# Optimization experiments

Hardware: AMD Instinct MI355X
Metric: run time of the kernel (lower is better)

## Reference

```python
import jax, jax.numpy as jnp
import numpy as np

N_HEADS = 8
D_HEAD = 64
INNER = N_HEADS * D_HEAD  # 512
D_X = 512
D_CTX = 768

def setup_inputs() -> dict:
    key = jax.random.key(0)
    ks = jax.random.split(key, 7)
    x = jax.random.normal(ks[0], (4, 4096, D_X), dtype=jnp.float32)
    context = jax.random.normal(ks[1], (4, 1024, D_CTX), dtype=jnp.float32)
    # Glorot-ish scaled params
    Wq = jax.random.normal(ks[2], (D_X, INNER), dtype=jnp.float32) / np.sqrt(D_X)
    Wk = jax.random.normal(ks[3], (D_CTX, INNER), dtype=jnp.float32) / np.sqrt(D_CTX)
    Wv = jax.random.normal(ks[4], (D_CTX, INNER), dtype=jnp.float32) / np.sqrt(D_CTX)
    Wo = jax.random.normal(ks[5], (INNER, INNER), dtype=jnp.float32) / np.sqrt(INNER)
    bo = jnp.zeros((INNER,), dtype=jnp.float32)
    return {"x": x, "context": context, "Wq": Wq, "Wk": Wk, "Wv": Wv, "Wo": Wo, "bo": bo}

def reference(x, context, Wq, Wk, Wv, Wo, bo):
    B, Nq, _ = x.shape
    Nc = context.shape[1]
    scale = D_HEAD ** -0.5
    # QKV projections (no bias), reshape to heads: b s (h d) -> b h s d
    q = (x @ Wq).reshape(B, Nq, N_HEADS, D_HEAD).transpose(0, 2, 1, 3)
    k = (context @ Wk).reshape(B, Nc, N_HEADS, D_HEAD).transpose(0, 2, 1, 3)
    v = (context @ Wv).reshape(B, Nc, N_HEADS, D_HEAD).transpose(0, 2, 1, 3)
    # scores: [B, H, Nq, Nc]
    score = jnp.einsum('bhqd,bhkd->bhqk', q, k) * scale
    weights = jax.nn.softmax(score, axis=-1)
    attn = jnp.einsum('bhqk,bhkd->bhqd', weights, v)
    out = attn.transpose(0, 2, 1, 3).reshape(B, Nq, INNER)
    return out @ Wo + bo
```

## Files before the change

### kernel.cpp

```cpp
#include <hip/hip_runtime.h>
#include <math.h>

typedef __attribute__((ext_vector_type(8))) short s8v;
typedef __attribute__((ext_vector_type(4))) float f4v;
typedef unsigned short u16;
typedef unsigned int u32;

constexpr int Bsz = 4, NQ = 4096, NC = 1024, NH = 8, DH = 64, DI = 512, DC = 768;

__device__ __forceinline__ u16 f2bf(float f) {
  union { float f; u32 u; } v; v.f = f;
  u32 r = v.u + 0x7fff + ((v.u >> 16) & 1);
  return (u16)(r >> 16);
}

__device__ __forceinline__ u32 pack2(float a, float b) {
  union { float f; u32 u; } ua, ub; ua.f = a; ub.f = b;
#if __has_builtin(__builtin_amdgcn_perm)
  return __builtin_amdgcn_perm(ub.u + 0x8000u, ua.u + 0x8000u, 0x07060302u);
#else
  return ((ub.u + 0x8000u) & 0xffff0000u) | ((ua.u + 0x8000u) >> 16);
#endif
}

__device__ __forceinline__ u32 cvtpk(float a, float b) {
  u32 r;
  asm("v_cvt_pk_bf16_f32 %0, %1, %2" : "=v"(r) : "v"(a), "v"(b));
  return r;
}

#if __has_builtin(__builtin_amdgcn_exp2f)
#define EXP2(x) __builtin_amdgcn_exp2f(x)
#else
#define EXP2(x) exp2f(x)
#endif

__device__ __forceinline__ void g2l16(const void* g, void* l) {
  __builtin_amdgcn_global_load_lds((const __attribute__((address_space(1))) u32*)g,
                                   (__attribute__((address_space(3))) u32*)l, 16, 0, 0);
}

__global__ __launch_bounds__(256) void prep(const float* __restrict__ Wq, const float* __restrict__ Wk,
                                            const float* __restrict__ Wv, const float* __restrict__ Wo,
                                            u16* __restrict__ wqT, u16* __restrict__ wkvT,
                                            u16* __restrict__ woT) {
  int idx = blockIdx.x;
  int z = idx / 96, rem = idx % 96, kx = rem % 12, ny = rem / 12;
  const float* src; u16* dst; int K; const int N = 512;
  if (z == 0)      { src = Wq; dst = wqT;              K = 512; }
  else if (z == 1) { src = Wk; dst = wkvT;             K = 768; }
  else if (z == 2) { src = Wv; dst = wkvT + 512 * 768; K = 768; }
  else             { src = Wo; dst = woT;              K = 512; }
  int k0 = kx * 64, n0 = ny * 64;
  if (k0 >= K) return;
  __shared__ u16 t[64][65];
  int tid = threadIdx.x, jr = tid & 63, ir = tid >> 6;
  for (int it = 0; it < 16; ++it) { int i = it * 4 + ir; t[i][jr] = f2bf(src[(size_t)(k0 + i) * N + n0 + jr]); }
  __syncthreads();
  for (int it = 0; it < 16; ++it) { int i = it * 4 + ir; dst[(size_t)(n0 + i) * K + k0 + jr] = t[jr][i]; }
}

template <int MODE, bool F32A>
__device__ __forceinline__ void gemm_body(const void* __restrict__ Av, const u16* __restrict__ Bt,
                                          void* __restrict__ C0, void* __restrict__ C1,
                                          const float* __restrict__ bias, int N, int K,
                                          float oscale, int nbx, int mby,
                                          u16* Al, u16* Bl) {
  int mb = mby * 128, nb = nbx * 128;
  int tid = threadIdx.x, lane = tid & 63, quad = lane >> 4, l16 = lane & 15, wave = tid >> 6;
  int wm = (wave >> 1) * 64, wn = (wave & 1) * 64;
  f4v acc[4][4];
  #pragma unroll
  for (int i = 0; i < 4; i++)
    #pragma unroll
    for (int j = 0; j < 4; j++) acc[i][j] = (f4v){0.f, 0.f, 0.f, 0.f};

  int r0 = tid >> 2;
  int cs = ((tid & 3) ^ ((r0 >> 1) & 3)) * 8;
  int lin = tid * 8;
  const u16* Bp0 = Bt + (size_t)(nb + r0) * K + cs;
  const u16* Bp1 = Bp0 + (size_t)64 * K;
  const float* Af0 = nullptr; const float* Af1 = nullptr;
  const u16* Ap0 = nullptr; const u16* Ap1 = nullptr;
  if constexpr (F32A) {
    Af0 = (const float*)Av + (size_t)(mb + r0) * K + cs;
    Af1 = Af0 + (size_t)64 * K;
  } else {
    Ap0 = (const u16*)Av + (size_t)(mb + r0) * K + cs;
    Ap1 = Ap0 + (size_t)64 * K;
  }
  float4 ra[4], rb[4];

#define BSTG(k0, bl_) do { g2l16(Bp0 + (k0), (bl_) + lin); g2l16(Bp1 + (k0), (bl_) + lin + 2048); } while (0)
#define ASTG(k0, al_) do { g2l16(Ap0 + (k0), (al_) + lin); g2l16(Ap1 + (k0), (al_) + lin + 2048); } while (0)
#define ALD(k0, s) do { \
    s[0] = *(const float4*)(Af0 + (k0)); s[1] = *(const float4*)(Af0 + (k0) + 4); \
    s[2] = *(const float4*)(Af1 + (k0)); s[3] = *(const float4*)(Af1 + (k0) + 4); } while (0)
#define AWR(s, al_) do { union { u32 d[4]; s8v v; } ua, ub; \
    ua.d[0] = cvtpk(s[0].x, s[0].y); ua.d[1] = cvtpk(s[0].z, s[0].w); \
    ua.d[2] = cvtpk(s[1].x, s[1].y); ua.d[3] = cvtpk(s[1].z, s[1].w); \
    ub.d[0] = cvtpk(s[2].x, s[2].y); ub.d[1] = cvtpk(s[2].z, s[2].w); \
    ub.d[2] = cvtpk(s[3].x, s[3].y); ub.d[3] = cvtpk(s[3].z, s[3].w); \
    *(s8v*)((al_) + lin) = ua.v; *(s8v*)((al_) + lin + 2048) = ub.v; } while (0)

  u16 *Ar = Al, *Aw = Al + 4096, *As = Al + 8192;
  u16 *Br = Bl, *Bw = Bl + 4096, *Bs = Bl + 8192;
  if constexpr (F32A) {
    ALD(0, ra); BSTG(0, Br); AWR(ra, Ar);
    ALD(32, rb); BSTG(32, Bw);
  } else {
    ASTG(0, Ar); BSTG(0, Br);
    ASTG(32, Aw); BSTG(32, Bw);
  }

  int nk = K >> 5;
  int swq8 = (quad ^ ((l16 >> 1) & 3)) * 8;
  for (int t = 0; t < nk; ++t) {
    if (t + 1 < nk) {
      if constexpr (F32A) asm volatile("s_waitcnt vmcnt(6) lgkmcnt(0)" ::: "memory");
      else                asm volatile("s_waitcnt vmcnt(4) lgkmcnt(0)" ::: "memory");
    } else {
      asm volatile("s_waitcnt vmcnt(0) lgkmcnt(0)" ::: "memory");
    }
    __builtin_amdgcn_s_barrier();
    asm volatile("" ::: "memory");
    __builtin_amdgcn_sched_barrier(0);

    if (t + 2 < nk) {
      int nxt = (t + 2) * 32;
      if constexpr (F32A) {
        if (t & 1) { ALD(nxt, rb); } else { ALD(nxt, ra); }
        BSTG(nxt, Bs);
      } else {
        ASTG(nxt, As); BSTG(nxt, Bs);
      }
    }

    s8v af[4], bfr[4];
    #pragma unroll
    for (int i = 0; i < 4; i++) af[i] = *(const s8v*)(Ar + (wm + i * 16 + l16) * 32 + swq8);
    #pragma unroll
    for (int j = 0; j < 4; j++) bfr[j] = *(const s8v*)(Br + (wn + j * 16 + l16) * 32 + swq8);
    #pragma unroll
    for (int i = 0; i < 4; i++)
      #pragma unroll
      for (int j = 0; j < 4; j++)
        acc[i][j] = __builtin_amdgcn_mfma_f32_16x16x32_bf16(af[i], bfr[j], acc[i][j], 0, 0, 0);

    if constexpr (F32A) {
      if (t + 1 < nk) {
        if (t & 1) { AWR(ra, Aw); } else { AWR(rb, Aw); }
      }
    }
    u16* tA = Ar; Ar = Aw; Aw = As; As = tA;
    u16* tB = Br; Br = Bw; Bw = Bs; Bs = tB;
  }
#undef BSTG
#undef ASTG
#undef ALD
#undef AWR
  #pragma unroll
  for (int i = 0; i < 4; i++) {
    int rbase = mb + wm + i * 16 + quad * 4;
    #pragma unroll
    for (int j = 0; j < 4; j++) {
      int col = nb + wn + j * 16 + l16;
      if (MODE == 0) {
        u16* Cb = (u16*)C0;
        #pragma unroll
        for (int r = 0; r < 4; r++) Cb[(size_t)(rbase + r) * N + col] = f2bf(acc[i][j][r] * oscale);
      } else if (MODE == 1) {
        float* Cf = (float*)C0;
        #pragma unroll
        for (int r = 0; r < 4; r++) Cf[(size_t)(rbase + r) * N + col] = acc[i][j][r] + bias[col];
      } else {
        if (col < 512) {
          u16* Kb = (u16*)C0;
          #pragma unroll
          for (int r = 0; r < 4; r++) Kb[(size_t)(rbase + r) * 512 + col] = f2bf(acc[i][j][r]);
        } else {
          u16* Vt = (u16*)C1;
          int hd = col - 512, h = hd >> 6, d = hd & 63;
          int bb = rbase >> 10, tl = rbase & 1023;
          int tbase = tl & ~63, a0 = tl & 63;
          int pb = (a0 & 32) + ((a0 & 15) >> 2) * 8 + (((a0 >> 4) & 1) << 2);
          uint2 ov;
          ov.x = pack2(acc[i][j][0], acc[i][j][1]);
          ov.y = pack2(acc[i][j][2], acc[i][j][3]);
          *(uint2*)(Vt + ((size_t)(bb * NH + h) * DH + d) * NC + tbase + pb) = ov;
        }
      }
    }
  }
}

__global__ __launch_bounds__(256, 3) void proj_all(const float* __restrict__ x, const float* __restrict__ ctx,
                                                   const u16* __restrict__ wqT, const u16* __restrict__ wkvT,
                                                   u16* __restrict__ Qb, u16* __restrict__ Kb,
                                                   u16* __restrict__ Vtb, float qscale) {
  __shared__ alignas(16) u16 Al[3][128][32];
  __shared__ alignas(16) u16 Bl[3][128][32];
  int bx = blockIdx.x;
  int xcd = bx & 7, off = bx >> 3;
  if (off < 32) {
    int bi = xcd * 32 + off;
    gemm_body<2, true>(ctx, wkvT, Kb, Vtb, nullptr, 1024, 768, 1.0f, bi & 7, bi >> 3,
                       (u16*)Al, (u16*)Bl);
  } else {
    int bi = xcd * 64 + (off - 32);
    gemm_body<0, true>(x, wqT, Qb, nullptr, nullptr, 512, 512, qscale, bi & 3, bi >> 2,
                       (u16*)Al, (u16*)Bl);
  }
}

__global__ __launch_bounds__(256, 3) void outproj(const u16* __restrict__ Ob, const u16* __restrict__ woT,
                                                  float* __restrict__ out, const float* __restrict__ bo) {
  __shared__ alignas(16) u16 Al[3][128][32];
  __shared__ alignas(16) u16 Bl[3][128][32];
  int bx = blockIdx.x;
  int idx = (bx & 7) * 64 + (bx >> 3);
  gemm_body<1, false>(Ob, woT, out, nullptr, bo, 512, 512, 1.0f, idx & 3, idx >> 2,
                      (u16*)Al, (u16*)Bl);
}

__global__ __launch_bounds__(256, 4) void attn(const u16* __restrict__ Q, const u16* __restrict__ Kb,
                                               const u16* __restrict__ Vt, u16* __restrict__ O) {
  __shared__ alignas(16) u16 Kl[2][64][64];
  __shared__ alignas(16) u16 Vl[2][64][64];
  int qt = blockIdx.x, h = blockIdx.y, b = blockIdx.z;
  int tid = threadIdx.x, wave = tid >> 6, lane = tid & 63, quad = lane >> 4, l16 = lane & 15;
  int q0 = qt * 128 + wave * 32;
  int x7 = l16 & 7;

  int kr = tid >> 3, kc = (tid & 7) ^ (kr & 7);
  const u16* kg = Kb + ((size_t)b * NC + kr) * 512 + h * DH + kc * 8;
  const u16* vg = Vt + ((size_t)(b * NH + h) * DH + kr) * NC + kc * 8;

#define ASTAGE(kt, buf) do { \
    const u16* kg_ = kg + (size_t)(kt) * 64 * 512; \
    const u16* vg_ = vg + (kt) * 64; \
    u16* kl_ = (u16*)Kl + (buf) * 4096; u16* vl_ = (u16*)Vl + (buf) * 4096; \
    g2l16(kg_,            kl_ + tid * 8); \
    g2l16(kg_ + 32 * 512, kl_ + (tid + 256) * 8); \
    g2l16(vg_,            vl_ + tid * 8); \
    g2l16(vg_ + 32 * NC,  vl_ + (tid + 256) * 8); } while (0)

  s8v aq[2][2];
  {
    const u16* Qp = Q + ((size_t)b * NQ + q0 + l16) * DI + h * DH + quad * 8;
    #pragma unroll
    for (int n = 0; n < 2; n++) {
      aq[n][0] = *(const s8v*)(Qp + (size_t)n * 16 * DI);
      aq[n][1] = *(const s8v*)(Qp + (size_t)n * 16 * DI + 32);
    }
  }
  s8v vones;
  #pragma unroll
  for (int i = 0; i < 8; i++) vones[i] = (short)0x3F80;

  f4v oacc[4][2];
  f4v lacc[2];
  #pragma unroll
  for (int d = 0; d < 4; d++)
    #pragma unroll
    for (int n = 0; n < 2; n++) oacc[d][n] = (f4v){0.f, 0.f, 0.f, 0.f};
  #pragma unroll
  for (int n = 0; n < 2; n++) lacc[n] = (f4v){0.f, 0.f, 0.f, 0.f};

  ASTAGE(0, 0);
  for (int kt = 0; kt < NC / 64; ++kt) {
    int buf = kt & 1;
    __syncthreads();
    if (kt + 1 < NC / 64) ASTAGE(kt + 1, buf ^ 1);
    const u16* kb = (const u16*)Kl + buf * 4096;
    const u16* vb = (const u16*)Vl + buf * 4096;

    f4v S0[2][2], S1[2][2];
    #pragma unroll
    for (int mi = 0; mi < 2; mi++)
      #pragma unroll
      for (int n = 0; n < 2; n++) { S0[mi][n] = (f4v){0.f,0.f,0.f,0.f}; S1[mi][n] = (f4v){0.f,0.f,0.f,0.f}; }
    __builtin_amdgcn_s_setprio(1);
    #pragma unroll
    for (int cd = 0; cd < 2; cd++) {
      int ch = ((4 * cd + quad) ^ x7) * 8;
      s8v k00 = *(const s8v*)(kb + (l16     ) * 64 + ch);
      s8v k01 = *(const s8v*)(kb + (l16 + 16) * 64 + ch);
      #pragma unroll
      for (int n = 0; n < 2; n++) {
        S0[0][n] = __builtin_amdgcn_mfma_f32_16x16x32_bf16(k00, aq[n][cd], S0[0][n], 0, 0, 0);
        S0[1][n] = __builtin_amdgcn_mfma_f32_16x16x32_bf16(k01, aq[n][cd], S0[1][n], 0, 0, 0);
      }
      s8v k10 = *(const s8v*)(kb + (l16 + 32) * 64 + ch);
      s8v k11 = *(const s8v*)(kb + (l16 + 48) * 64 + ch);
      #pragma unroll
      for (int n = 0; n < 2; n++) {
        S1[0][n] = __builtin_amdgcn_mfma_f32_16x16x32_bf16(k10, aq[n][cd], S1[0][n], 0, 0, 0);
        S1[1][n] = __builtin_amdgcn_mfma_f32_16x16x32_bf16(k11, aq[n][cd], S1[1][n], 0, 0, 0);
      }
    }
    __builtin_amdgcn_s_setprio(0);

    s8v pf0[2];
    #pragma unroll
    for (int n = 0; n < 2; n++) {
      float p00 = EXP2(S0[0][n][0]), p01 = EXP2(S0[0][n][1]), p02 = EXP2(S0[0][n][2]), p03 = EXP2(S0[0][n][3]);
      float p10 = EXP2(S0[1][n][0]), p11 = EXP2(S0[1][n][1]), p12 = EXP2(S0[1][n][2]), p13 = EXP2(S0[1][n][3]);
      union { u32 d[4]; s8v v; } u;
      u.d[0] = cvtpk(p00, p01); u.d[1] = cvtpk(p02, p03);
      u.d[2] = cvtpk(p10, p11); u.d[3] = cvtpk(p12, p13);
      pf0[n] = u.v;
    }
    __builtin_amdgcn_s_setprio(1);
    #pragma unroll
    for (int n = 0; n < 2; n++)
      lacc[n] = __builtin_amdgcn_mfma_f32_16x16x32_bf16(vones, pf0[n], lacc[n], 0, 0, 0);
    #pragma unroll
    for (int d = 0; d < 4; d++) {
      int ch = (quad ^ x7) * 8;
      s8v vf = *(const s8v*)(vb + (d * 16 + l16) * 64 + ch);
      #pragma unroll
      for (int n = 0; n < 2; n++)
        oacc[d][n] = __builtin_amdgcn_mfma_f32_16x16x32_bf16(vf, pf0[n], oacc[d][n], 0, 0, 0);
    }
    __builtin_amdgcn_s_setprio(0);

    s8v pf1[2];
    #pragma unroll
    for (int n = 0; n < 2; n++) {
      float p00 = EXP2(S1[0][n][0]), p01 = EXP2(S1[0][n][1]), p02 = EXP2(S1[0][n][2]), p03 = EXP2(S1[0][n][3]);
      float p10 = EXP2(S1[1][n][0]), p11 = EXP2(S1[1][n][1]), p12 = EXP2(S1[1][n][2]), p13 = EXP2(S1[1][n][3]);
      union { u32 d[4]; s8v v; } u;
      u.d[0] = cvtpk(p00, p01); u.d[1] = cvtpk(p02, p03);
      u.d[2] = cvtpk(p10, p11); u.d[3] = cvtpk(p12, p13);
      pf1[n] = u.v;
    }
    __builtin_amdgcn_s_setprio(1);
    #pragma unroll
    for (int n = 0; n < 2; n++)
      lacc[n] = __builtin_amdgcn_mfma_f32_16x16x32_bf16(vones, pf1[n], lacc[n], 0, 0, 0);
    #pragma unroll
    for (int d = 0; d < 4; d++) {
      int ch = ((4 + quad) ^ x7) * 8;
      s8v vf = *(const s8v*)(vb + (d * 16 + l16) * 64 + ch);
      #pragma unroll
      for (int n = 0; n < 2; n++)
        oacc[d][n] = __builtin_amdgcn_mfma_f32_16x16x32_bf16(vf, pf1[n], oacc[d][n], 0, 0, 0);
    }
    __builtin_amdgcn_s_setprio(0);
  }
#undef ASTAGE

  float inv[2];
  #pragma unroll
  for (int n = 0; n < 2; n++) inv[n] = 1.0f / lacc[n][0];

  #pragma unroll
  for (int d = 0; d < 4; d++)
    #pragma unroll
    for (int n = 0; n < 2; n++) {
      int q = q0 + n * 16 + l16;
      uint2 ov;
      ov.x = cvtpk(oacc[d][n][0] * inv[n], oacc[d][n][1] * inv[n]);
      ov.y = cvtpk(oacc[d][n][2] * inv[n], oacc[d][n][3] * inv[n]);
      *(uint2*)(O + ((size_t)b * NQ + q) * DI + h * DH + d * 16 + quad * 4) = ov;
    }
}

extern "C" void kernel_launch(void* const* d_in, const int* in_sizes, int n_in,
                              void* d_out, int out_size, void* d_ws, size_t ws_size,
                              hipStream_t stream) {
  const float* x   = (const float*)d_in[0];
  const float* ctx = (const float*)d_in[1];
  const float* Wq  = (const float*)d_in[2];
  const float* Wk  = (const float*)d_in[3];
  const float* Wv  = (const float*)d_in[4];
  const float* Wo  = (const float*)d_in[5];
  const float* bo  = (const float*)d_in[6];
  float* out = (float*)d_out;

  u16* w    = (u16*)d_ws;
  u16* wqT  = w;
  u16* wkvT = wqT  + 262144;
  u16* woT  = wkvT + 786432;
  u16* Qb   = woT  + 262144;
  u16* Kbuf = Qb   + 8388608;
  u16* Vtb  = Kbuf + 2097152;
  u16* Ob   = Vtb  + 2097152;

  const float qscale = 0.125f * 1.44269504f;

  prep<<<384, 256, 0, stream>>>(Wq, Wk, Wv, Wo, wqT, wkvT, woT);
  proj_all<<<768, 256, 0, stream>>>(x, ctx, wqT, wkvT, Qb, Kbuf, Vtb, qscale);
  attn<<<dim3(32, 8, 4), 256, 0, stream>>>(Qb, Kbuf, Vtb, Ob);
  outproj<<<512, 256, 0, stream>>>(Ob, woT, out, bo);
}
```

Measured before the change: 188.6 us.

## Widen projection GEMM tiles to 128x256 so A reuses across two column tiles

The shared GEMM body now computes a 128x256 output tile per block instead of 128x128. Each wave holds two accumulator sets and stages four B row-chunks per k-step, so each converted A tile (including the fp32-to-bf16 conversion of x and context) feeds twice as many MFMAs. Grid sizes for the projection and output kernels are halved, and launch bounds drop from 3 to 2 blocks per CU to make room for the larger register and LDS footprint. The trade is fewer blocks in flight (384 and 256 on a large-CU GPU) and lower occupancy in exchange for less redundant A loading and conversion.

```diff
diff --git a/kernel.cpp b/kernel.cpp
--- a/kernel.cpp
+++ b/kernel.cpp
@@ -66,20 +66,24 @@
                                           const float* __restrict__ bias, int N, int K,
                                           float oscale, int nbx, int mby,
                                           u16* Al, u16* Bl) {
-  int mb = mby * 128, nb = nbx * 128;
+  int mb = mby * 128, nb = nbx * 256;
   int tid = threadIdx.x, lane = tid & 63, quad = lane >> 4, l16 = lane & 15, wave = tid >> 6;
   int wm = (wave >> 1) * 64, wn = (wave & 1) * 64;
-  f4v acc[4][4];
-  #pragma unroll
-  for (int i = 0; i < 4; i++)
-    #pragma unroll
-    for (int j = 0; j < 4; j++) acc[i][j] = (f4v){0.f, 0.f, 0.f, 0.f};
+  f4v acc[2][4][4];
+  #pragma unroll
+  for (int ct = 0; ct < 2; ct++)
+    #pragma unroll
+    for (int i = 0; i < 4; i++)
+      #pragma unroll
+      for (int j = 0; j < 4; j++) acc[ct][i][j] = (f4v){0.f, 0.f, 0.f, 0.f};
 
   int r0 = tid >> 2;
   int cs = ((tid & 3) ^ ((r0 >> 1) & 3)) * 8;
   int lin = tid * 8;
   const u16* Bp0 = Bt + (size_t)(nb + r0) * K + cs;
   const u16* Bp1 = Bp0 + (size_t)64 * K;
+  const u16* Bp2 = Bp0 + (size_t)128 * K;
+  const u16* Bp3 = Bp0 + (size_t)192 * K;
   const float* Af0 = nullptr; const float* Af1 = nullptr;
   const u16* Ap0 = nullptr; const u16* Ap1 = nullptr;
   if constexpr (F32A) {
@@ -91,7 +95,9 @@
   }
   float4 ra[4], rb[4];
 
-#define BSTG(k0, bl_) do { g2l16(Bp0 + (k0), (bl_) + lin); g2l16(Bp1 + (k0), (bl_) + lin + 2048); } while (0)
+#define BSTG(k0, bl_) do { \
+    g2l16(Bp0 + (k0), (bl_) + lin);        g2l16(Bp1 + (k0), (bl_) + lin + 2048); \
+    g2l16(Bp2 + (k0), (bl_) + lin + 4096); g2l16(Bp3 + (k0), (bl_) + lin + 6144); } while (0)
 #define ASTG(k0, al_) do { g2l16(Ap0 + (k0), (al_) + lin); g2l16(Ap1 + (k0), (al_) + lin + 2048); } while (0)
 #define ALD(k0, s) do { \
     s[0] = *(const float4*)(Af0 + (k0)); s[1] = *(const float4*)(Af0 + (k0) + 4); \
@@ -104,7 +110,7 @@
     *(s8v*)((al_) + lin) = ua.v; *(s8v*)((al_) + lin + 2048) = ub.v; } while (0)
 
   u16 *Ar = Al, *Aw = Al + 4096, *As = Al + 8192;
-  u16 *Br = Bl, *Bw = Bl + 4096, *Bs = Bl + 8192;
+  u16 *Br = Bl, *Bw = Bl + 8192, *Bs = Bl + 16384;
   if constexpr (F32A) {
     ALD(0, ra); BSTG(0, Br); AWR(ra, Ar);
     ALD(32, rb); BSTG(32, Bw);
@@ -117,8 +123,8 @@
   int swq8 = (quad ^ ((l16 >> 1) & 3)) * 8;
   for (int t = 0; t < nk; ++t) {
     if (t + 1 < nk) {
-      if constexpr (F32A) asm volatile("s_waitcnt vmcnt(6) lgkmcnt(0)" ::: "memory");
-      else                asm volatile("s_waitcnt vmcnt(4) lgkmcnt(0)" ::: "memory");
+      if constexpr (F32A) asm volatile("s_waitcnt vmcnt(8) lgkmcnt(0)" ::: "memory");
+      else                asm volatile("s_waitcnt vmcnt(6) lgkmcnt(0)" ::: "memory");
     } else {
       asm volatile("s_waitcnt vmcnt(0) lgkmcnt(0)" ::: "memory");
     }
@@ -136,16 +142,21 @@
       }
     }
 
-    s8v af[4], bfr[4];
+    s8v af[4], bfr[2][4];
     #pragma unroll
     for (int i = 0; i < 4; i++) af[i] = *(const s8v*)(Ar + (wm + i * 16 + l16) * 32 + swq8);
     #pragma unroll
-    for (int j = 0; j < 4; j++) bfr[j] = *(const s8v*)(Br + (wn + j * 16 + l16) * 32 + swq8);
-    #pragma unroll
-    for (int i = 0; i < 4; i++)
+    for (int ct = 0; ct < 2; ct++)
       #pragma unroll
       for (int j = 0; j < 4; j++)
-        acc[i][j] = __builtin_amdgcn_mfma_f32_16x16x32_bf16(af[i], bfr[j], acc[i][j], 0, 0, 0);
+        bfr[ct][j] = *(const s8v*)(Br + ct * 4096 + (wn + j * 16 + l16) * 32 + swq8);
+    #pragma unroll
+    for (int ct = 0; ct < 2; ct++)
+      #pragma unroll
+      for (int i = 0; i < 4; i++)
+        #pragma unroll
+        for (int j = 0; j < 4; j++)
+          acc[ct][i][j] = __builtin_amdgcn_mfma_f32_16x16x32_bf16(af[i], bfr[ct][j], acc[ct][i][j], 0, 0, 0);
 
     if constexpr (F32A) {
       if (t + 1 < nk) {
@@ -160,66 +171,69 @@
 #undef ALD
 #undef AWR
   #pragma unroll
-  for (int i = 0; i < 4; i++) {
-    int rbase = mb + wm + i * 16 + quad * 4;
-    #pragma unroll
-    for (int j = 0; j < 4; j++) {
-      int col = nb + wn + j * 16 + l16;
-      if (MODE == 0) {
-        u16* Cb = (u16*)C0;
-        #pragma unroll
-        for (int r = 0; r < 4; r++) Cb[(size_t)(rbase + r) * N + col] = f2bf(acc[i][j][r] * oscale);
-      } else if (MODE == 1) {
-        float* Cf = (float*)C0;
-        #pragma unroll
-        for (int r = 0; r < 4; r++) Cf[(size_t)(rbase + r) * N + col] = acc[i][j][r] + bias[col];
-      } else {
-        if (col < 512) {
-          u16* Kb = (u16*)C0;
+  for (int ct = 0; ct < 2; ct++) {
+    #pragma unroll
+    for (int i = 0; i < 4; i++) {
+      int rbase = mb + wm + i * 16 + quad * 4;
+      #pragma unroll
+      for (int j = 0; j < 4; j++) {
+        int col = nb + ct * 128 + wn + j * 16 + l16;
+        if (MODE == 0) {
+          u16* Cb = (u16*)C0;
           #pragma unroll
-          for (int r = 0; r < 4; r++) Kb[(size_t)(rbase + r) * 512 + col] = f2bf(acc[i][j][r]);
+          for (int r = 0; r < 4; r++) Cb[(size_t)(rbase + r) * N + col] = f2bf(acc[ct][i][j][r] * oscale);
+        } else if (MODE == 1) {
+          float* Cf = (float*)C0;
+          #pragma unroll
+          for (int r = 0; r < 4; r++) Cf[(size_t)(rbase + r) * N + col] = acc[ct][i][j][r] + bias[col];
         } else {
-          u16* Vt = (u16*)C1;
-          int hd = col - 512, h = hd >> 6, d = hd & 63;
-          int bb = rbase >> 10, tl = rbase & 1023;
-          int tbase = tl & ~63, a0 = tl & 63;
-          int pb = (a0 & 32) + ((a0 & 15) >> 2) * 8 + (((a0 >> 4) & 1) << 2);
-          uint2 ov;
-          ov.x = pack2(acc[i][j][0], acc[i][j][1]);
-          ov.y = pack2(acc[i][j][2], acc[i][j][3]);
-          *(uint2*)(Vt + ((size_t)(bb * NH + h) * DH + d) * NC + tbase + pb) = ov;
+          if (col < 512) {
+            u16* Kb = (u16*)C0;
+            #pragma unroll
+            for (int r = 0; r < 4; r++) Kb[(size_t)(rbase + r) * 512 + col] = f2bf(acc[ct][i][j][r]);
+          } else {
+            u16* Vt = (u16*)C1;
+            int hd = col - 512, h = hd >> 6, d = hd & 63;
+            int bb = rbase >> 10, tl = rbase & 1023;
+            int tbase = tl & ~63, a0 = tl & 63;
+            int pb = (a0 & 32) + ((a0 & 15) >> 2) * 8 + (((a0 >> 4) & 1) << 2);
+            uint2 ov;
+            ov.x = pack2(acc[ct][i][j][0], acc[ct][i][j][1]);
+            ov.y = pack2(acc[ct][i][j][2], acc[ct][i][j][3]);
+            *(uint2*)(Vt + ((size_t)(bb * NH + h) * DH + d) * NC + tbase + pb) = ov;
+          }
         }
       }
     }
   }
 }
 
-__global__ __launch_bounds__(256, 3) void proj_all(const float* __restrict__ x, const float* __restrict__ ctx,
+__global__ __launch_bounds__(256, 2) void proj_all(const float* __restrict__ x, const float* __restrict__ ctx,
                                                    const u16* __restrict__ wqT, const u16* __restrict__ wkvT,
                                                    u16* __restrict__ Qb, u16* __restrict__ Kb,
                                                    u16* __restrict__ Vtb, float qscale) {
   __shared__ alignas(16) u16 Al[3][128][32];
-  __shared__ alignas(16) u16 Bl[3][128][32];
+  __shared__ alignas(16) u16 Bl[3][2][128][32];
   int bx = blockIdx.x;
   int xcd = bx & 7, off = bx >> 3;
-  if (off < 32) {
-    int bi = xcd * 32 + off;
-    gemm_body<2, true>(ctx, wkvT, Kb, Vtb, nullptr, 1024, 768, 1.0f, bi & 7, bi >> 3,
+  if (off < 16) {
+    int bi = xcd * 16 + off;
+    gemm_body<2, true>(ctx, wkvT, Kb, Vtb, nullptr, 1024, 768, 1.0f, bi & 3, bi >> 2,
                        (u16*)Al, (u16*)Bl);
   } else {
-    int bi = xcd * 64 + (off - 32);
-    gemm_body<0, true>(x, wqT, Qb, nullptr, nullptr, 512, 512, qscale, bi & 3, bi >> 2,
+    int bi = xcd * 32 + (off - 16);
+    gemm_body<0, true>(x, wqT, Qb, nullptr, nullptr, 512, 512, qscale, bi & 1, bi >> 1,
                        (u16*)Al, (u16*)Bl);
   }
 }
 
-__global__ __launch_bounds__(256, 3) void outproj(const u16* __restrict__ Ob, const u16* __restrict__ woT,
+__global__ __launch_bounds__(256, 2) void outproj(const u16* __restrict__ Ob, const u16* __restrict__ woT,
                                                   float* __restrict__ out, const float* __restrict__ bo) {
   __shared__ alignas(16) u16 Al[3][128][32];
-  __shared__ alignas(16) u16 Bl[3][128][32];
+  __shared__ alignas(16) u16 Bl[3][2][128][32];
   int bx = blockIdx.x;
-  int idx = (bx & 7) * 64 + (bx >> 3);
-  gemm_body<1, false>(Ob, woT, out, nullptr, bo, 512, 512, 1.0f, idx & 3, idx >> 2,
+  int idx = (bx & 7) * 32 + (bx >> 3);
+  gemm_body<1, false>(Ob, woT, out, nullptr, bo, 512, 512, 1.0f, idx & 1, idx >> 1,
                       (u16*)Al, (u16*)Bl);
 }
 
@@ -391,7 +405,7 @@
   const float qscale = 0.125f * 1.44269504f;
 
   prep<<<384, 256, 0, stream>>>(Wq, Wk, Wv, Wo, wqT, wkvT, woT);
-  proj_all<<<768, 256, 0, stream>>>(x, ctx, wqT, wkvT, Qb, Kbuf, Vtb, qscale);
+  proj_all<<<384, 256, 0, stream>>>(x, ctx, wqT, wkvT, Qb, Kbuf, Vtb, qscale);
   attn<<<dim3(32, 8, 4), 256, 0, stream>>>(Qb, Kbuf, Vtb, Ob);
-  outproj<<<512, 256, 0, stream>>>(Ob, woT, out, bo);
-}
+  outproj<<<256, 256, 0, stream>>>(Ob, woT, out, bo);
+}
```

Result: no change. 187.5 us (-0.6%).
